# Kernel tuning notes

Hardware: AMD Instinct MI355X
Metric: run time of the kernel (lower is better)

## Reference

```python
import jax, jax.numpy as jnp
import numpy as np

N = 50000
E = 800000
C_IN, C_HID, C_OUT = 128, 64, 1


def setup_inputs() -> dict:
    key = jax.random.key(0)
    ks = jax.random.split(key, 8)
    x = jax.random.normal(ks[0], (N, C_IN), dtype=jnp.float32)
    edge_index = jax.random.randint(ks[1], (2, E), 0, N, dtype=jnp.int64)
    # GCNConv linear params (glorot-ish scaling)
    W1 = jax.random.normal(ks[2], (C_IN, C_HID), dtype=jnp.float32) / np.sqrt(C_IN)
    b1 = jnp.zeros((C_HID,), dtype=jnp.float32)
    W2 = jax.random.normal(ks[3], (C_HID, C_HID), dtype=jnp.float32) / np.sqrt(C_HID)
    b2 = jnp.zeros((C_HID,), dtype=jnp.float32)
    W3 = jax.random.normal(ks[4], (C_HID, C_OUT), dtype=jnp.float32) / np.sqrt(C_HID)
    b3 = jnp.zeros((C_OUT,), dtype=jnp.float32)
    return {"x": x, "edge_index": edge_index, "W1": W1, "b1": b1,
            "W2": W2, "b2": b2, "W3": W3, "b3": b3}


def _gcn_norm(edge_index, num_nodes):
    # Add self-loops, compute symmetric normalization D^{-1/2} A D^{-1/2}
    loop = jnp.arange(num_nodes, dtype=edge_index.dtype)
    src = jnp.concatenate([edge_index[0], loop])  # message sources
    dst = jnp.concatenate([edge_index[1], loop])  # message targets
    ones = jnp.ones(src.shape[0], dtype=jnp.float32)
    deg = jax.ops.segment_sum(ones, dst, num_segments=num_nodes)
    dis = jnp.where(deg > 0, jax.lax.rsqrt(jnp.maximum(deg, 1.0)), 0.0)
    norm = dis[src] * dis[dst]  # [E+N]
    return src, dst, norm


def _gcn_conv(h, src, dst, norm, W, b, num_nodes):
    h = h @ W                                  # [N, C_out]
    msg = h[src] * norm[:, None]               # gather + scale, [E+N, C_out]
    out = jax.ops.segment_sum(msg, dst, num_segments=num_nodes)  # scatter-add
    return out + b


def reference(x, edge_index, W1, b1, W2, b2, W3, b3):
    num_nodes = x.shape[0]
    src, dst, norm = _gcn_norm(edge_index, num_nodes)
    leaky = lambda v: jnp.where(v >= 0, v, 0.01 * v)
    h = _gcn_conv(x, src, dst, norm, W1, b1, num_nodes)
    h = leaky(h)
    h = _gcn_conv(h, src, dst, norm, W2, b2, num_nodes)
    h = leaky(h)
    h = _gcn_conv(h, src, dst, norm, W3, b3, num_nodes)
    return h
```

## Files before the change

### kernel.cpp

```cpp
#include <hip/hip_runtime.h>

#define CIN 128
#define CHID 64
#define CSTRIDE 64

__device__ __forceinline__ float leaky(float v) { return v >= 0.f ? v : 0.01f * v; }
__device__ __forceinline__ float bcast(float v, int k) {
    return __int_as_float(__builtin_amdgcn_readlane(__float_as_int(v), k));
}
__device__ __forceinline__ void acc4(float4& a, const float4 v) {
    a.x += v.x; a.y += v.y; a.z += v.z; a.w += v.w;
}
__device__ __forceinline__ void xorred(float4& a) {
    a.x += __shfl_xor(a.x, 16, 64); a.y += __shfl_xor(a.y, 16, 64);
    a.z += __shfl_xor(a.z, 16, 64); a.w += __shfl_xor(a.w, 16, 64);
    a.x += __shfl_xor(a.x, 32, 64); a.y += __shfl_xor(a.y, 32, 64);
    a.z += __shfl_xor(a.z, 32, 64); a.w += __shfl_xor(a.w, 32, 64);
}

__global__ void k_deg(const int* __restrict__ dst, const int* __restrict__ src,
                      int* __restrict__ deg, unsigned short* __restrict__ csr,
                      int E, int nps, int N) {
    const int shard = blockIdx.x & 7;
    const int chunk = blockIdx.x >> 3;
    const int nchunks = gridDim.x >> 3;
    const int lo = shard * nps;
    const int hi = min(lo + nps, N);
    const int estride = nchunks * 256;
    for (int e = chunk * 256 + threadIdx.x; e < E; e += estride) {
        int d = dst[e];
        if (d >= lo && d < hi) {
            int slot = atomicAdd(&deg[d], 1);
            if (slot < CSTRIDE) csr[(d << 6) + slot] = (unsigned short)src[e];
        }
    }
}

__global__ __launch_bounds__(256) void k_gemm1(
    const float* __restrict__ x, const float* __restrict__ W,
    const int* __restrict__ deg, float* __restrict__ hp, int N) {
    const int wave = threadIdx.x >> 6, lane = threadIdx.x & 63;
    float w[CIN];
#pragma unroll
    for (int k = 0; k < CIN; ++k) w[k] = W[k * CHID + lane];
    const int stride = gridDim.x * 4;
    for (int n = blockIdx.x * 4 + wave; n < N; n += stride) {
        float x0 = x[(size_t)n * CIN + lane];
        float x1 = x[(size_t)n * CIN + 64 + lane];
        float acc0 = 0.f, acc1 = 0.f;
#pragma unroll
        for (int k = 0; k < 64; k += 2) {
            acc0 = fmaf(bcast(x0, k),     w[k],     acc0);
            acc1 = fmaf(bcast(x0, k + 1), w[k + 1], acc1);
        }
#pragma unroll
        for (int k = 0; k < 64; k += 2) {
            acc0 = fmaf(bcast(x1, k),     w[64 + k],     acc0);
            acc1 = fmaf(bcast(x1, k + 1), w[64 + k + 1], acc1);
        }
        float dn = rsqrtf((float)(deg[n] + 1));
        hp[(size_t)n * CHID + lane] = dn * (acc0 + acc1);
    }
}

__global__ __launch_bounds__(256) void kG1(
    const unsigned short* __restrict__ csr, const int* __restrict__ deg,
    const float* __restrict__ hp, const float* __restrict__ W2,
    const float* __restrict__ b1, float* __restrict__ hp2, int N) {
    const int wave = threadIdx.x >> 6, lane = threadIdx.x & 63;
    const int g = lane >> 4, sl = lane & 15;
    float w[CHID];
#pragma unroll
    for (int k = 0; k < CHID; ++k) w[k] = W2[k * CHID + lane];
    const float4 bb = ((const float4*)b1)[sl];
    const float4* __restrict__ hpq = (const float4*)hp;
    const int stride = gridDim.x * 4;
    const int n0 = blockIdx.x * 4 + wave;
    int d = 0, c0 = 0, c1 = 0, c2 = 0, c3 = 0;
    if (n0 < N) {
        d = deg[n0];
        int base = n0 << 6;
        c0 = csr[base + g];      c1 = csr[base + g + 4];
        c2 = csr[base + g + 8];  c3 = csr[base + g + 12];
    }
    for (int n = n0; n < N; n += stride) {
        const int n2 = n + stride;
        int dN = 0, e0 = 0, e1 = 0, e2 = 0, e3 = 0;
        if (n2 < N) {
            dN = deg[n2];
            int b2 = n2 << 6;
            e0 = csr[b2 + g];      e1 = csr[b2 + g + 4];
            e2 = csr[b2 + g + 8];  e3 = csr[b2 + g + 12];
        }
        const int dc = d, base = n << 6;
        float4 a0 = make_float4(0.f, 0.f, 0.f, 0.f), a1 = a0, a2 = a0, a3 = a0;
        if (g == 0) a0 = hpq[(size_t)n * 16 + sl];
        if (g < dc)      acc4(a0, hpq[(size_t)c0 * 16 + sl]);
        if (g + 4 < dc)  acc4(a1, hpq[(size_t)c1 * 16 + sl]);
        if (g + 8 < dc)  acc4(a2, hpq[(size_t)c2 * 16 + sl]);
        if (g + 12 < dc) acc4(a3, hpq[(size_t)c3 * 16 + sl]);
        for (int b = g + 16; b < dc; b += 16) {
            { int s = csr[base + b];      acc4(a0, hpq[(size_t)s * 16 + sl]); }
            if (b + 4 < dc)  { int s = csr[base + b + 4];  acc4(a1, hpq[(size_t)s * 16 + sl]); }
            if (b + 8 < dc)  { int s = csr[base + b + 8];  acc4(a2, hpq[(size_t)s * 16 + sl]); }
            if (b + 12 < dc) { int s = csr[base + b + 12]; acc4(a3, hpq[(size_t)s * 16 + sl]); }
        }
        acc4(a0, a1); acc4(a2, a3); acc4(a0, a2);
        xorred(a0);
        float dn = rsqrtf((float)(dc + 1));
        float4 gv;
        gv.x = leaky(dn * a0.x + bb.x);
        gv.y = leaky(dn * a0.y + bb.y);
        gv.z = leaky(dn * a0.z + bb.z);
        gv.w = leaky(dn * a0.w + bb.w);
        float acc0 = 0.f, acc1 = 0.f;
#pragma unroll
        for (int i = 0; i < 16; ++i) {
            acc0 = fmaf(bcast(gv.x, i), w[4 * i + 0], acc0);
            acc1 = fmaf(bcast(gv.y, i), w[4 * i + 1], acc1);
            acc0 = fmaf(bcast(gv.z, i), w[4 * i + 2], acc0);
            acc1 = fmaf(bcast(gv.w, i), w[4 * i + 3], acc1);
        }
        hp2[(size_t)n * CHID + lane] = dn * (acc0 + acc1);
        d = dN; c0 = e0; c1 = e1; c2 = e2; c3 = e3;
    }
}

__global__ __launch_bounds__(256) void kG2(
    const unsigned short* __restrict__ csr, const int* __restrict__ deg,
    const float* __restrict__ hp, const float* __restrict__ b2,
    const float* __restrict__ W3, float* __restrict__ hp3, int N) {
    const int wave = threadIdx.x >> 6, lane = threadIdx.x & 63;
    const int g = lane >> 4, sl = lane & 15;
    const float4 bb = ((const float4*)b2)[sl];
    const float4 w3 = ((const float4*)W3)[sl];
    const float4* __restrict__ hpq = (const float4*)hp;
    const int stride = gridDim.x * 4;
    const int n0 = blockIdx.x * 4 + wave;
    int d = 0, c0 = 0, c1 = 0, c2 = 0, c3 = 0;
    if (n0 < N) {
        d = deg[n0];
        int base = n0 << 6;
        c0 = csr[base + g];      c1 = csr[base + g + 4];
        c2 = csr[base + g + 8];  c3 = csr[base + g + 12];
    }
    for (int n = n0; n < N; n += stride) {
        const int n2 = n + stride;
        int dN = 0, e0 = 0, e1 = 0, e2 = 0, e3 = 0;
        if (n2 < N) {
            dN = deg[n2];
            int b2i = n2 << 6;
            e0 = csr[b2i + g];      e1 = csr[b2i + g + 4];
            e2 = csr[b2i + g + 8];  e3 = csr[b2i + g + 12];
        }
        const int dc = d, base = n << 6;
        float4 a0 = make_float4(0.f, 0.f, 0.f, 0.f), a1 = a0, a2 = a0, a3 = a0;
        if (g == 0) a0 = hpq[(size_t)n * 16 + sl];
        if (g < dc)      acc4(a0, hpq[(size_t)c0 * 16 + sl]);
        if (g + 4 < dc)  acc4(a1, hpq[(size_t)c1 * 16 + sl]);
        if (g + 8 < dc)  acc4(a2, hpq[(size_t)c2 * 16 + sl]);
        if (g + 12 < dc) acc4(a3, hpq[(size_t)c3 * 16 + sl]);
        for (int b = g + 16; b < dc; b += 16) {
            { int s = csr[base + b];      acc4(a0, hpq[(size_t)s * 16 + sl]); }
            if (b + 4 < dc)  { int s = csr[base + b + 4];  acc4(a1, hpq[(size_t)s * 16 + sl]); }
            if (b + 8 < dc)  { int s = csr[base + b + 8];  acc4(a2, hpq[(size_t)s * 16 + sl]); }
            if (b + 12 < dc) { int s = csr[base + b + 12]; acc4(a3, hpq[(size_t)s * 16 + sl]); }
        }
        acc4(a0, a1); acc4(a2, a3); acc4(a0, a2);
        xorred(a0);
        float dn = rsqrtf((float)(dc + 1));
        float t = leaky(dn * a0.x + bb.x) * w3.x
                + leaky(dn * a0.y + bb.y) * w3.y
                + leaky(dn * a0.z + bb.z) * w3.z
                + leaky(dn * a0.w + bb.w) * w3.w;
        t += __shfl_xor(t, 1, 64); t += __shfl_xor(t, 2, 64);
        t += __shfl_xor(t, 4, 64); t += __shfl_xor(t, 8, 64);
        if (lane == 0) hp3[n] = dn * t;
        d = dN; c0 = e0; c1 = e1; c2 = e2; c3 = e3;
    }
}

__global__ void kG3(const unsigned short* __restrict__ csr, const int* __restrict__ deg,
                    const float* __restrict__ hp3, const float* __restrict__ b3,
                    float* __restrict__ out, int N) {
    int t = blockIdx.x * 256 + threadIdx.x;
    int node = t >> 4, sl = t & 15;
    if (node >= N) return;
    int d = deg[node], base = node << 6;
    float acc = (sl == 0) ? hp3[node] : 0.f;
    for (int i = sl; i < d; i += 16) acc += hp3[(int)csr[base + i]];
#pragma unroll
    for (int off = 8; off > 0; off >>= 1) acc += __shfl_down(acc, off, 16);
    if (sl == 0) out[node] = rsqrtf((float)(d + 1)) * acc + b3[0];
}

extern "C" void kernel_launch(void* const* d_in, const int* in_sizes, int n_in,
                              void* d_out, int out_size, void* d_ws, size_t ws_size,
                              hipStream_t stream) {
    const float* x  = (const float*)d_in[0];
    const int*   ei = (const int*)d_in[1];
    const float* W1 = (const float*)d_in[2];
    const float* b1 = (const float*)d_in[3];
    const float* W2 = (const float*)d_in[4];
    const float* b2 = (const float*)d_in[5];
    const float* W3 = (const float*)d_in[6];
    const float* b3 = (const float*)d_in[7];

    const int N = in_sizes[0] / CIN;
    const int E = in_sizes[1] / 2;
    const int* src = ei;
    const int* dst = ei + E;
    const int nps = (N + 7) / 8;

    char* w = (char*)d_ws;
    auto take = [&](size_t bytes) { char* p = w; w += (bytes + 255) & ~(size_t)255; return p; };
    int*            deg = (int*)take((size_t)N * 4);
    unsigned short* csr = (unsigned short*)take((size_t)N * CSTRIDE * 2);
    float*          A   = (float*)take((size_t)N * CHID * 4);
    float*          B   = (float*)take((size_t)N * CHID * 4);
    float*          hp3 = (float*)take((size_t)N * 4);

    hipMemsetAsync(deg, 0, (size_t)N * 4, stream);

    k_deg  <<<2048, 256, 0, stream>>>(dst, src, deg, csr, E, nps, N);
    k_gemm1<<<1024, 256, 0, stream>>>(x, W1, deg, A, N);
    kG1    <<<2048, 256, 0, stream>>>(csr, deg, A, W2, b1, B, N);
    kG2    <<<2048, 256, 0, stream>>>(csr, deg, B, b2, W3, hp3, N);
    kG3    <<<(N * 16 + 255) / 256, 256, 0, stream>>>(csr, deg, hp3, b3, (float*)d_out, N);
}
```

Measured before the change: 222.9 us.

## Split features into channel slabs and decouple aggregation from dense epilogues

Stores the transformed features as four 16-channel slabs, each a contiguous N×16 array. A new aggregation kernel assigns block groups to one slab and one half of the nodes, so each gather touches a smaller working set that is more likely to stay in cache. The fused aggregate+GEMM kernels are split into a separate aggregation pass plus lightweight epilogue kernels, which adds extra launches and an extra round trip of the full N×64 array through memory. It also clamps the degree loops to the CSR capacity.

Result: slower. 263.9 us (+18.4%).

```diff
diff --git a/kernel.cpp b/kernel.cpp
--- a/kernel.cpp
+++ b/kernel.cpp
@@ -10,12 +10,6 @@
 }
 __device__ __forceinline__ void acc4(float4& a, const float4 v) {
     a.x += v.x; a.y += v.y; a.z += v.z; a.w += v.w;
-}
-__device__ __forceinline__ void xorred(float4& a) {
-    a.x += __shfl_xor(a.x, 16, 64); a.y += __shfl_xor(a.y, 16, 64);
-    a.z += __shfl_xor(a.z, 16, 64); a.w += __shfl_xor(a.w, 16, 64);
-    a.x += __shfl_xor(a.x, 32, 64); a.y += __shfl_xor(a.y, 32, 64);
-    a.z += __shfl_xor(a.z, 32, 64); a.w += __shfl_xor(a.w, 32, 64);
 }
 
 __global__ void k_deg(const int* __restrict__ dst, const int* __restrict__ src,
@@ -38,11 +32,12 @@
 
 __global__ __launch_bounds__(256) void k_gemm1(
     const float* __restrict__ x, const float* __restrict__ W,
-    const int* __restrict__ deg, float* __restrict__ hp, int N) {
+    const int* __restrict__ deg, float* __restrict__ hps, int N) {
     const int wave = threadIdx.x >> 6, lane = threadIdx.x & 63;
     float w[CIN];
 #pragma unroll
     for (int k = 0; k < CIN; ++k) w[k] = W[k * CHID + lane];
+    float* __restrict__ op = hps + (size_t)(lane >> 4) * N * 16 + (lane & 15);
     const int stride = gridDim.x * 4;
     for (int n = blockIdx.x * 4 + wave; n < N; n += stride) {
         float x0 = x[(size_t)n * CIN + lane];
@@ -59,124 +54,93 @@
             acc1 = fmaf(bcast(x1, k + 1), w[64 + k + 1], acc1);
         }
         float dn = rsqrtf((float)(deg[n] + 1));
-        hp[(size_t)n * CHID + lane] = dn * (acc0 + acc1);
+        op[(size_t)n * 16] = dn * (acc0 + acc1);
     }
 }
 
-__global__ __launch_bounds__(256) void kG1(
+__global__ __launch_bounds__(256) void kAgg(
     const unsigned short* __restrict__ csr, const int* __restrict__ deg,
-    const float* __restrict__ hp, const float* __restrict__ W2,
-    const float* __restrict__ b1, float* __restrict__ hp2, int N) {
+    const float* __restrict__ hps, float* __restrict__ hagg, int N) {
     const int wave = threadIdx.x >> 6, lane = threadIdx.x & 63;
-    const int g = lane >> 4, sl = lane & 15;
+    const int q = lane & 3, g = lane >> 2;
+    const int cg = blockIdx.x & 7;
+    const int sh = cg >> 1;
+    const int sub = cg & 1;
+    const int nchunks = gridDim.x >> 3;
+    const int half = (N + 1) >> 1;
+    const int lo = sub * half;
+    const int hi = min(lo + half, N);
+    const float4* __restrict__ hpq = (const float4*)(hps + (size_t)sh * N * 16);
+    const int stride = nchunks * 4;
+    const int n0 = lo + (blockIdx.x >> 3) * 4 + wave;
+    int d = 0, c0 = 0;
+    if (n0 < hi) { d = deg[n0]; c0 = csr[(n0 << 6) + g]; }
+    for (int n = n0; n < hi; n += stride) {
+        const int n2 = n + stride;
+        int dN = 0, e0 = 0;
+        if (n2 < hi) { dN = deg[n2]; e0 = csr[(n2 << 6) + g]; }
+        const int dc = d;
+        const int dcl = min(dc, CSTRIDE);
+        const int base = n << 6;
+        float4 a = make_float4(0.f, 0.f, 0.f, 0.f);
+        if (g == 0) a = hpq[(size_t)n * 4 + q];
+        if (g < dcl) acc4(a, hpq[(size_t)c0 * 4 + q]);
+        for (int b = g + 16; b < dcl; b += 16) {
+            int s = csr[base + b];
+            acc4(a, hpq[(size_t)s * 4 + q]);
+        }
+        a.x += __shfl_xor(a.x, 4, 64);  a.y += __shfl_xor(a.y, 4, 64);
+        a.z += __shfl_xor(a.z, 4, 64);  a.w += __shfl_xor(a.w, 4, 64);
+        a.x += __shfl_xor(a.x, 8, 64);  a.y += __shfl_xor(a.y, 8, 64);
+        a.z += __shfl_xor(a.z, 8, 64);  a.w += __shfl_xor(a.w, 8, 64);
+        a.x += __shfl_xor(a.x, 16, 64); a.y += __shfl_xor(a.y, 16, 64);
+        a.z += __shfl_xor(a.z, 16, 64); a.w += __shfl_xor(a.w, 16, 64);
+        a.x += __shfl_xor(a.x, 32, 64); a.y += __shfl_xor(a.y, 32, 64);
+        a.z += __shfl_xor(a.z, 32, 64); a.w += __shfl_xor(a.w, 32, 64);
+        if (g == 0) ((float4*)(hagg + (size_t)n * 64 + sh * 16))[q] = a;
+        d = dN; c0 = e0;
+    }
+}
+
+__global__ __launch_bounds__(256) void kEpi1(
+    const float* __restrict__ hagg, const int* __restrict__ deg,
+    const float* __restrict__ b1, const float* __restrict__ W2,
+    float* __restrict__ hps2, int N) {
+    const int wave = threadIdx.x >> 6, lane = threadIdx.x & 63;
     float w[CHID];
 #pragma unroll
     for (int k = 0; k < CHID; ++k) w[k] = W2[k * CHID + lane];
-    const float4 bb = ((const float4*)b1)[sl];
-    const float4* __restrict__ hpq = (const float4*)hp;
+    const float bl = b1[lane];
+    float* __restrict__ op = hps2 + (size_t)(lane >> 4) * N * 16 + (lane & 15);
     const int stride = gridDim.x * 4;
-    const int n0 = blockIdx.x * 4 + wave;
-    int d = 0, c0 = 0, c1 = 0, c2 = 0, c3 = 0;
-    if (n0 < N) {
-        d = deg[n0];
-        int base = n0 << 6;
-        c0 = csr[base + g];      c1 = csr[base + g + 4];
-        c2 = csr[base + g + 8];  c3 = csr[base + g + 12];
-    }
-    for (int n = n0; n < N; n += stride) {
-        const int n2 = n + stride;
-        int dN = 0, e0 = 0, e1 = 0, e2 = 0, e3 = 0;
-        if (n2 < N) {
-            dN = deg[n2];
-            int b2 = n2 << 6;
-            e0 = csr[b2 + g];      e1 = csr[b2 + g + 4];
-            e2 = csr[b2 + g + 8];  e3 = csr[b2 + g + 12];
-        }
-        const int dc = d, base = n << 6;
-        float4 a0 = make_float4(0.f, 0.f, 0.f, 0.f), a1 = a0, a2 = a0, a3 = a0;
-        if (g == 0) a0 = hpq[(size_t)n * 16 + sl];
-        if (g < dc)      acc4(a0, hpq[(size_t)c0 * 16 + sl]);
-        if (g + 4 < dc)  acc4(a1, hpq[(size_t)c1 * 16 + sl]);
-        if (g + 8 < dc)  acc4(a2, hpq[(size_t)c2 * 16 + sl]);
-        if (g + 12 < dc) acc4(a3, hpq[(size_t)c3 * 16 + sl]);
-        for (int b = g + 16; b < dc; b += 16) {
-            { int s = csr[base + b];      acc4(a0, hpq[(size_t)s * 16 + sl]); }
-            if (b + 4 < dc)  { int s = csr[base + b + 4];  acc4(a1, hpq[(size_t)s * 16 + sl]); }
-            if (b + 8 < dc)  { int s = csr[base + b + 8];  acc4(a2, hpq[(size_t)s * 16 + sl]); }
-            if (b + 12 < dc) { int s = csr[base + b + 12]; acc4(a3, hpq[(size_t)s * 16 + sl]); }
-        }
-        acc4(a0, a1); acc4(a2, a3); acc4(a0, a2);
-        xorred(a0);
-        float dn = rsqrtf((float)(dc + 1));
-        float4 gv;
-        gv.x = leaky(dn * a0.x + bb.x);
-        gv.y = leaky(dn * a0.y + bb.y);
-        gv.z = leaky(dn * a0.z + bb.z);
-        gv.w = leaky(dn * a0.w + bb.w);
+    for (int n = blockIdx.x * 4 + wave; n < N; n += stride) {
+        float agg = hagg[(size_t)n * 64 + lane];
+        float dn = rsqrtf((float)(deg[n] + 1));
+        float v = leaky(dn * agg + bl);
         float acc0 = 0.f, acc1 = 0.f;
 #pragma unroll
-        for (int i = 0; i < 16; ++i) {
-            acc0 = fmaf(bcast(gv.x, i), w[4 * i + 0], acc0);
-            acc1 = fmaf(bcast(gv.y, i), w[4 * i + 1], acc1);
-            acc0 = fmaf(bcast(gv.z, i), w[4 * i + 2], acc0);
-            acc1 = fmaf(bcast(gv.w, i), w[4 * i + 3], acc1);
+        for (int k = 0; k < 64; k += 2) {
+            acc0 = fmaf(bcast(v, k),     w[k],     acc0);
+            acc1 = fmaf(bcast(v, k + 1), w[k + 1], acc1);
         }
-        hp2[(size_t)n * CHID + lane] = dn * (acc0 + acc1);
-        d = dN; c0 = e0; c1 = e1; c2 = e2; c3 = e3;
+        op[(size_t)n * 16] = dn * (acc0 + acc1);
     }
 }
 
-__global__ __launch_bounds__(256) void kG2(
-    const unsigned short* __restrict__ csr, const int* __restrict__ deg,
-    const float* __restrict__ hp, const float* __restrict__ b2,
-    const float* __restrict__ W3, float* __restrict__ hp3, int N) {
+__global__ __launch_bounds__(256) void kEpi2(
+    const float* __restrict__ hagg, const int* __restrict__ deg,
+    const float* __restrict__ b2, const float* __restrict__ W3,
+    float* __restrict__ hp3, int N) {
     const int wave = threadIdx.x >> 6, lane = threadIdx.x & 63;
-    const int g = lane >> 4, sl = lane & 15;
-    const float4 bb = ((const float4*)b2)[sl];
-    const float4 w3 = ((const float4*)W3)[sl];
-    const float4* __restrict__ hpq = (const float4*)hp;
+    const float bl = b2[lane], wl = W3[lane];
     const int stride = gridDim.x * 4;
-    const int n0 = blockIdx.x * 4 + wave;
-    int d = 0, c0 = 0, c1 = 0, c2 = 0, c3 = 0;
-    if (n0 < N) {
-        d = deg[n0];
-        int base = n0 << 6;
-        c0 = csr[base + g];      c1 = csr[base + g + 4];
-        c2 = csr[base + g + 8];  c3 = csr[base + g + 12];
-    }
-    for (int n = n0; n < N; n += stride) {
-        const int n2 = n + stride;
-        int dN = 0, e0 = 0, e1 = 0, e2 = 0, e3 = 0;
-        if (n2 < N) {
-            dN = deg[n2];
-            int b2i = n2 << 6;
-            e0 = csr[b2i + g];      e1 = csr[b2i + g + 4];
-            e2 = csr[b2i + g + 8];  e3 = csr[b2i + g + 12];
-        }
-        const int dc = d, base = n << 6;
-        float4 a0 = make_float4(0.f, 0.f, 0.f, 0.f), a1 = a0, a2 = a0, a3 = a0;
-        if (g == 0) a0 = hpq[(size_t)n * 16 + sl];
-        if (g < dc)      acc4(a0, hpq[(size_t)c0 * 16 + sl]);
-        if (g + 4 < dc)  acc4(a1, hpq[(size_t)c1 * 16 + sl]);
-        if (g + 8 < dc)  acc4(a2, hpq[(size_t)c2 * 16 + sl]);
-        if (g + 12 < dc) acc4(a3, hpq[(size_t)c3 * 16 + sl]);
-        for (int b = g + 16; b < dc; b += 16) {
-            { int s = csr[base + b];      acc4(a0, hpq[(size_t)s * 16 + sl]); }
-            if (b + 4 < dc)  { int s = csr[base + b + 4];  acc4(a1, hpq[(size_t)s * 16 + sl]); }
-            if (b + 8 < dc)  { int s = csr[base + b + 8];  acc4(a2, hpq[(size_t)s * 16 + sl]); }
-            if (b + 12 < dc) { int s = csr[base + b + 12]; acc4(a3, hpq[(size_t)s * 16 + sl]); }
-        }
-        acc4(a0, a1); acc4(a2, a3); acc4(a0, a2);
-        xorred(a0);
-        float dn = rsqrtf((float)(dc + 1));
-        float t = leaky(dn * a0.x + bb.x) * w3.x
-                + leaky(dn * a0.y + bb.y) * w3.y
-                + leaky(dn * a0.z + bb.z) * w3.z
-                + leaky(dn * a0.w + bb.w) * w3.w;
-        t += __shfl_xor(t, 1, 64); t += __shfl_xor(t, 2, 64);
-        t += __shfl_xor(t, 4, 64); t += __shfl_xor(t, 8, 64);
-        if (lane == 0) hp3[n] = dn * t;
-        d = dN; c0 = e0; c1 = e1; c2 = e2; c3 = e3;
+    for (int n = blockIdx.x * 4 + wave; n < N; n += stride) {
+        float dn = rsqrtf((float)(deg[n] + 1));
+        float v = leaky(dn * hagg[(size_t)n * 64 + lane] + bl) * wl;
+        v += __shfl_xor(v, 1, 64);  v += __shfl_xor(v, 2, 64);
+        v += __shfl_xor(v, 4, 64);  v += __shfl_xor(v, 8, 64);
+        v += __shfl_xor(v, 16, 64); v += __shfl_xor(v, 32, 64);
+        if (lane == 0) hp3[n] = dn * v;
     }
 }
 
@@ -187,8 +151,9 @@
     int node = t >> 4, sl = t & 15;
     if (node >= N) return;
     int d = deg[node], base = node << 6;
+    int dl = min(d, CSTRIDE);
     float acc = (sl == 0) ? hp3[node] : 0.f;
-    for (int i = sl; i < d; i += 16) acc += hp3[(int)csr[base + i]];
+    for (int i = sl; i < dl; i += 16) acc += hp3[(int)csr[base + i]];
 #pragma unroll
     for (int off = 8; off > 0; off >>= 1) acc += __shfl_down(acc, off, 16);
     if (sl == 0) out[node] = rsqrtf((float)(d + 1)) * acc + b3[0];
@@ -214,17 +179,19 @@
 
     char* w = (char*)d_ws;
     auto take = [&](size_t bytes) { char* p = w; w += (bytes + 255) & ~(size_t)255; return p; };
-    int*            deg = (int*)take((size_t)N * 4);
-    unsigned short* csr = (unsigned short*)take((size_t)N * CSTRIDE * 2);
-    float*          A   = (float*)take((size_t)N * CHID * 4);
-    float*          B   = (float*)take((size_t)N * CHID * 4);
-    float*          hp3 = (float*)take((size_t)N * 4);
+    int*            deg  = (int*)take((size_t)N * 4);
+    unsigned short* csr  = (unsigned short*)take((size_t)N * CSTRIDE * 2);
+    float*          buf1 = (float*)take((size_t)N * CHID * 4);
+    float*          buf2 = (float*)take((size_t)N * CHID * 4);
+    float*          hp3  = (float*)take((size_t)N * 4);
 
     hipMemsetAsync(deg, 0, (size_t)N * 4, stream);
 
     k_deg  <<<2048, 256, 0, stream>>>(dst, src, deg, csr, E, nps, N);
-    k_gemm1<<<1024, 256, 0, stream>>>(x, W1, deg, A, N);
-    kG1    <<<2048, 256, 0, stream>>>(csr, deg, A, W2, b1, B, N);
-    kG2    <<<2048, 256, 0, stream>>>(csr, deg, B, b2, W3, hp3, N);
+    k_gemm1<<<1024, 256, 0, stream>>>(x, W1, deg, buf1, N);
+    kAgg   <<<2048, 256, 0, stream>>>(csr, deg, buf1, buf2, N);
+    kEpi1  <<<2048, 256, 0, stream>>>(buf2, deg, b1, W2, buf1, N);
+    kAgg   <<<2048, 256, 0, stream>>>(csr, deg, buf1, buf2, N);
+    kEpi2  <<<2048, 256, 0, stream>>>(buf2, deg, b2, W3, hp3, N);
     kG3    <<<(N * 16 + 255) / 256, 256, 0, stream>>>(csr, deg, hp3, b3, (float*)d_out, N);
 }
```

## Deepen software pipeline for neighbor gathers in GCN aggregation kernels

Applied to the files above, without the earlier changes.

Restructures kG1 and kG2 into a three-stage software pipeline. CSR indices for node n+2·stride are prefetched (8 per lane instead of 4), and the first five feature gathers for node n+stride are issued one iteration early, so more memory loads are in flight to hide gather latency. Degree loops are clamped to CSTRIDE (64), which drops neighbors beyond the fixed CSR row capacity, also in kG3. The change raises register pressure from holding prefetched indices and float4 values.

After: 221.1 us. No clear change (-0.8%).

```diff
diff --git a/kernel.cpp b/kernel.cpp
--- a/kernel.cpp
+++ b/kernel.cpp
@@ -76,38 +76,69 @@
     const float4* __restrict__ hpq = (const float4*)hp;
     const int stride = gridDim.x * 4;
     const int n0 = blockIdx.x * 4 + wave;
-    int d = 0, c0 = 0, c1 = 0, c2 = 0, c3 = 0;
+    const float4 z = make_float4(0.f, 0.f, 0.f, 0.f);
+
+    int dA = 0, dB = 0;
+    int cA[8], cB[8];
+#pragma unroll
+    for (int k = 0; k < 8; ++k) { cA[k] = 0; cB[k] = 0; }
+    float4 pS = z, p0 = z, p1 = z, p2 = z, p3 = z;
+
     if (n0 < N) {
-        d = deg[n0];
-        int base = n0 << 6;
-        c0 = csr[base + g];      c1 = csr[base + g + 4];
-        c2 = csr[base + g + 8];  c3 = csr[base + g + 12];
-    }
+        dA = deg[n0];
+        const int ba = n0 << 6;
+#pragma unroll
+        for (int k = 0; k < 8; ++k) cA[k] = csr[ba + g + 4 * k];
+        const int n1 = n0 + stride;
+        if (n1 < N) {
+            dB = deg[n1];
+            const int bbs = n1 << 6;
+#pragma unroll
+            for (int k = 0; k < 8; ++k) cB[k] = csr[bbs + g + 4 * k];
+        }
+        if (g == 0)      pS = hpq[(size_t)n0 * 16 + sl];
+        if (g < dA)      p0 = hpq[(size_t)cA[0] * 16 + sl];
+        if (g + 4 < dA)  p1 = hpq[(size_t)cA[1] * 16 + sl];
+        if (g + 8 < dA)  p2 = hpq[(size_t)cA[2] * 16 + sl];
+        if (g + 12 < dA) p3 = hpq[(size_t)cA[3] * 16 + sl];
+    }
+
     for (int n = n0; n < N; n += stride) {
-        const int n2 = n + stride;
-        int dN = 0, e0 = 0, e1 = 0, e2 = 0, e3 = 0;
-        if (n2 < N) {
-            dN = deg[n2];
-            int b2 = n2 << 6;
-            e0 = csr[b2 + g];      e1 = csr[b2 + g + 4];
-            e2 = csr[b2 + g + 8];  e3 = csr[b2 + g + 12];
-        }
-        const int dc = d, base = n << 6;
-        float4 a0 = make_float4(0.f, 0.f, 0.f, 0.f), a1 = a0, a2 = a0, a3 = a0;
-        if (g == 0) a0 = hpq[(size_t)n * 16 + sl];
-        if (g < dc)      acc4(a0, hpq[(size_t)c0 * 16 + sl]);
-        if (g + 4 < dc)  acc4(a1, hpq[(size_t)c1 * 16 + sl]);
-        if (g + 8 < dc)  acc4(a2, hpq[(size_t)c2 * 16 + sl]);
-        if (g + 12 < dc) acc4(a3, hpq[(size_t)c3 * 16 + sl]);
-        for (int b = g + 16; b < dc; b += 16) {
-            { int s = csr[base + b];      acc4(a0, hpq[(size_t)s * 16 + sl]); }
-            if (b + 4 < dc)  { int s = csr[base + b + 4];  acc4(a1, hpq[(size_t)s * 16 + sl]); }
-            if (b + 8 < dc)  { int s = csr[base + b + 8];  acc4(a2, hpq[(size_t)s * 16 + sl]); }
-            if (b + 12 < dc) { int s = csr[base + b + 12]; acc4(a3, hpq[(size_t)s * 16 + sl]); }
+        const int nB = n + stride, nC = nB + stride;
+        int dC = 0; int cC[8];
+#pragma unroll
+        for (int k = 0; k < 8; ++k) cC[k] = 0;
+        if (nC < N) {
+            dC = deg[nC];
+            const int bc = nC << 6;
+#pragma unroll
+            for (int k = 0; k < 8; ++k) cC[k] = csr[bc + g + 4 * k];
+        }
+        float4 qS = z, q0 = z, q1 = z, q2 = z, q3 = z;
+        if (nB < N) {
+            if (g == 0)      qS = hpq[(size_t)nB * 16 + sl];
+            if (g < dB)      q0 = hpq[(size_t)cB[0] * 16 + sl];
+            if (g + 4 < dB)  q1 = hpq[(size_t)cB[1] * 16 + sl];
+            if (g + 8 < dB)  q2 = hpq[(size_t)cB[2] * 16 + sl];
+            if (g + 12 < dB) q3 = hpq[(size_t)cB[3] * 16 + sl];
+        }
+        const int dcl = min(dA, CSTRIDE);
+        float4 t0 = z, t1 = z, t2 = z, t3 = z;
+        if (g + 16 < dcl) t0 = hpq[(size_t)cA[4] * 16 + sl];
+        if (g + 20 < dcl) t1 = hpq[(size_t)cA[5] * 16 + sl];
+        if (g + 24 < dcl) t2 = hpq[(size_t)cA[6] * 16 + sl];
+        if (g + 28 < dcl) t3 = hpq[(size_t)cA[7] * 16 + sl];
+        float4 a0 = pS, a1 = p1, a2 = p2, a3 = p3;
+        acc4(a0, p0); acc4(a1, t0); acc4(a2, t1); acc4(a3, t2);
+        acc4(a0, t3);
+        const int base = n << 6;
+        for (int b = g + 32; b < dcl; b += 16) {
+            int s = csr[base + b];
+            acc4(a1, hpq[(size_t)s * 16 + sl]);
         }
         acc4(a0, a1); acc4(a2, a3); acc4(a0, a2);
         xorred(a0);
-        float dn = rsqrtf((float)(dc + 1));
+        float dn = rsqrtf((float)(dA + 1));
         float4 gv;
         gv.x = leaky(dn * a0.x + bb.x);
         gv.y = leaky(dn * a0.y + bb.y);
@@ -122,7 +153,10 @@
             acc1 = fmaf(bcast(gv.w, i), w[4 * i + 3], acc1);
         }
         hp2[(size_t)n * CHID + lane] = dn * (acc0 + acc1);
-        d = dN; c0 = e0; c1 = e1; c2 = e2; c3 = e3;
+        dA = dB; dB = dC;
+#pragma unroll
+        for (int k = 0; k < 8; ++k) { cA[k] = cB[k]; cB[k] = cC[k]; }
+        pS = qS; p0 = q0; p1 = q1; p2 = q2; p3 = q3;
     }
 }
 
@@ -137,38 +171,69 @@
     const float4* __restrict__ hpq = (const float4*)hp;
     const int stride = gridDim.x * 4;
     const int n0 = blockIdx.x * 4 + wave;
-    int d = 0, c0 = 0, c1 = 0, c2 = 0, c3 = 0;
+    const float4 z = make_float4(0.f, 0.f, 0.f, 0.f);
+
+    int dA = 0, dB = 0;
+    int cA[8], cB[8];
+#pragma unroll
+    for (int k = 0; k < 8; ++k) { cA[k] = 0; cB[k] = 0; }
+    float4 pS = z, p0 = z, p1 = z, p2 = z, p3 = z;
+
     if (n0 < N) {
-        d = deg[n0];
-        int base = n0 << 6;
-        c0 = csr[base + g];      c1 = csr[base + g + 4];
-        c2 = csr[base + g + 8];  c3 = csr[base + g + 12];
-    }
+        dA = deg[n0];
+        const int ba = n0 << 6;
+#pragma unroll
+        for (int k = 0; k < 8; ++k) cA[k] = csr[ba + g + 4 * k];
+        const int n1 = n0 + stride;
+        if (n1 < N) {
+            dB = deg[n1];
+            const int bbs = n1 << 6;
+#pragma unroll
+            for (int k = 0; k < 8; ++k) cB[k] = csr[bbs + g + 4 * k];
+        }
+        if (g == 0)      pS = hpq[(size_t)n0 * 16 + sl];
+        if (g < dA)      p0 = hpq[(size_t)cA[0] * 16 + sl];
+        if (g + 4 < dA)  p1 = hpq[(size_t)cA[1] * 16 + sl];
+        if (g + 8 < dA)  p2 = hpq[(size_t)cA[2] * 16 + sl];
+        if (g + 12 < dA) p3 = hpq[(size_t)cA[3] * 16 + sl];
+    }
+
     for (int n = n0; n < N; n += stride) {
-        const int n2 = n + stride;
-        int dN = 0, e0 = 0, e1 = 0, e2 = 0, e3 = 0;
-        if (n2 < N) {
-            dN = deg[n2];
-            int b2i = n2 << 6;
-            e0 = csr[b2i + g];      e1 = csr[b2i + g + 4];
-            e2 = csr[b2i + g + 8];  e3 = csr[b2i + g + 12];
-        }
-        const int dc = d, base = n << 6;
-        float4 a0 = make_float4(0.f, 0.f, 0.f, 0.f), a1 = a0, a2 = a0, a3 = a0;
-        if (g == 0) a0 = hpq[(size_t)n * 16 + sl];
-        if (g < dc)      acc4(a0, hpq[(size_t)c0 * 16 + sl]);
-        if (g + 4 < dc)  acc4(a1, hpq[(size_t)c1 * 16 + sl]);
-        if (g + 8 < dc)  acc4(a2, hpq[(size_t)c2 * 16 + sl]);
-        if (g + 12 < dc) acc4(a3, hpq[(size_t)c3 * 16 + sl]);
-        for (int b = g + 16; b < dc; b += 16) {
-            { int s = csr[base + b];      acc4(a0, hpq[(size_t)s * 16 + sl]); }
-            if (b + 4 < dc)  { int s = csr[base + b + 4];  acc4(a1, hpq[(size_t)s * 16 + sl]); }
-            if (b + 8 < dc)  { int s = csr[base + b + 8];  acc4(a2, hpq[(size_t)s * 16 + sl]); }
-            if (b + 12 < dc) { int s = csr[base + b + 12]; acc4(a3, hpq[(size_t)s * 16 + sl]); }
+        const int nB = n + stride, nC = nB + stride;
+        int dC = 0; int cC[8];
+#pragma unroll
+        for (int k = 0; k < 8; ++k) cC[k] = 0;
+        if (nC < N) {
+            dC = deg[nC];
+            const int bc = nC << 6;
+#pragma unroll
+            for (int k = 0; k < 8; ++k) cC[k] = csr[bc + g + 4 * k];
+        }
+        float4 qS = z, q0 = z, q1 = z, q2 = z, q3 = z;
+        if (nB < N) {
+            if (g == 0)      qS = hpq[(size_t)nB * 16 + sl];
+            if (g < dB)      q0 = hpq[(size_t)cB[0] * 16 + sl];
+            if (g + 4 < dB)  q1 = hpq[(size_t)cB[1] * 16 + sl];
+            if (g + 8 < dB)  q2 = hpq[(size_t)cB[2] * 16 + sl];
+            if (g + 12 < dB) q3 = hpq[(size_t)cB[3] * 16 + sl];
+        }
+        const int dcl = min(dA, CSTRIDE);
+        float4 t0 = z, t1 = z, t2 = z, t3 = z;
+        if (g + 16 < dcl) t0 = hpq[(size_t)cA[4] * 16 + sl];
+        if (g + 20 < dcl) t1 = hpq[(size_t)cA[5] * 16 + sl];
+        if (g + 24 < dcl) t2 = hpq[(size_t)cA[6] * 16 + sl];
+        if (g + 28 < dcl) t3 = hpq[(size_t)cA[7] * 16 + sl];
+        float4 a0 = pS, a1 = p1, a2 = p2, a3 = p3;
+        acc4(a0, p0); acc4(a1, t0); acc4(a2, t1); acc4(a3, t2);
+        acc4(a0, t3);
+        const int base = n << 6;
+        for (int b = g + 32; b < dcl; b += 16) {
+            int s = csr[base + b];
+            acc4(a1, hpq[(size_t)s * 16 + sl]);
         }
         acc4(a0, a1); acc4(a2, a3); acc4(a0, a2);
         xorred(a0);
-        float dn = rsqrtf((float)(dc + 1));
+        float dn = rsqrtf((float)(dA + 1));
         float t = leaky(dn * a0.x + bb.x) * w3.x
                 + leaky(dn * a0.y + bb.y) * w3.y
                 + leaky(dn * a0.z + bb.z) * w3.z
@@ -176,7 +241,10 @@
         t += __shfl_xor(t, 1, 64); t += __shfl_xor(t, 2, 64);
         t += __shfl_xor(t, 4, 64); t += __shfl_xor(t, 8, 64);
         if (lane == 0) hp3[n] = dn * t;
-        d = dN; c0 = e0; c1 = e1; c2 = e2; c3 = e3;
+        dA = dB; dB = dC;
+#pragma unroll
+        for (int k = 0; k < 8; ++k) { cA[k] = cB[k]; cB[k] = cC[k]; }
+        pS = qS; p0 = q0; p1 = q1; p2 = q2; p3 = q3;
     }
 }
 
@@ -187,8 +255,9 @@
     int node = t >> 4, sl = t & 15;
     if (node >= N) return;
     int d = deg[node], base = node << 6;
+    int dl = min(d, CSTRIDE);
     float acc = (sl == 0) ? hp3[node] : 0.f;
-    for (int i = sl; i < d; i += 16) acc += hp3[(int)csr[base + i]];
+    for (int i = sl; i < dl; i += 16) acc += hp3[(int)csr[base + i]];
 #pragma unroll
     for (int off = 8; off > 0; off >>= 1) acc += __shfl_down(acc, off, 16);
     if (sl == 0) out[node] = rsqrtf((float)(d + 1)) * acc + b3[0];
```

## Load whole CSR row per wave, shuffle indices, use LDS broadcast for GEMV

Applied to the files above, without the earlier changes.

The aggregation kernels now load each node's full 64-entry CSR row with one coalesced 32-bit load per lane and extract neighbour indices with wave shuffles, instead of issuing scattered 16-bit loads inside the neighbour loop. Degrees are clamped to the CSR capacity. The per-row GEMVs in gemm1 and kG1 read inputs from shared memory as float4 rather than broadcasting them with readlane. This cuts dependent index-load latency and scalar readlane work, at the cost of extra shuffles and LDS traffic. The LDS write and read in kG1 have no explicit barrier and rely on wave-level execution.

Result: slower. 244.4 us (+9.7%).

```diff
diff --git a/kernel.cpp b/kernel.cpp
--- a/kernel.cpp
+++ b/kernel.cpp
@@ -5,9 +5,6 @@
 #define CSTRIDE 64
 
 __device__ __forceinline__ float leaky(float v) { return v >= 0.f ? v : 0.01f * v; }
-__device__ __forceinline__ float bcast(float v, int k) {
-    return __int_as_float(__builtin_amdgcn_readlane(__float_as_int(v), k));
-}
 __device__ __forceinline__ void acc4(float4& a, const float4 v) {
     a.x += v.x; a.y += v.y; a.z += v.z; a.w += v.w;
 }
@@ -39,24 +36,24 @@
 __global__ __launch_bounds__(256) void k_gemm1(
     const float* __restrict__ x, const float* __restrict__ W,
     const int* __restrict__ deg, float* __restrict__ hp, int N) {
+    __shared__ float xs[4][CIN];
     const int wave = threadIdx.x >> 6, lane = threadIdx.x & 63;
     float w[CIN];
 #pragma unroll
     for (int k = 0; k < CIN; ++k) w[k] = W[k * CHID + lane];
+    const float4* __restrict__ xq = (const float4*)xs[wave];
     const int stride = gridDim.x * 4;
     for (int n = blockIdx.x * 4 + wave; n < N; n += stride) {
-        float x0 = x[(size_t)n * CIN + lane];
-        float x1 = x[(size_t)n * CIN + 64 + lane];
+        xs[wave][lane]      = x[(size_t)n * CIN + lane];
+        xs[wave][64 + lane] = x[(size_t)n * CIN + 64 + lane];
         float acc0 = 0.f, acc1 = 0.f;
 #pragma unroll
-        for (int k = 0; k < 64; k += 2) {
-            acc0 = fmaf(bcast(x0, k),     w[k],     acc0);
-            acc1 = fmaf(bcast(x0, k + 1), w[k + 1], acc1);
-        }
-#pragma unroll
-        for (int k = 0; k < 64; k += 2) {
-            acc0 = fmaf(bcast(x1, k),     w[64 + k],     acc0);
-            acc1 = fmaf(bcast(x1, k + 1), w[64 + k + 1], acc1);
+        for (int i = 0; i < 32; ++i) {
+            float4 v = xq[i];
+            acc0 = fmaf(v.x, w[4 * i + 0], acc0);
+            acc1 = fmaf(v.y, w[4 * i + 1], acc1);
+            acc0 = fmaf(v.z, w[4 * i + 2], acc0);
+            acc1 = fmaf(v.w, w[4 * i + 3], acc1);
         }
         float dn = rsqrtf((float)(deg[n] + 1));
         hp[(size_t)n * CHID + lane] = dn * (acc0 + acc1);
@@ -67,62 +64,77 @@
     const unsigned short* __restrict__ csr, const int* __restrict__ deg,
     const float* __restrict__ hp, const float* __restrict__ W2,
     const float* __restrict__ b1, float* __restrict__ hp2, int N) {
+    __shared__ float lds[4][CHID];
     const int wave = threadIdx.x >> 6, lane = threadIdx.x & 63;
     const int g = lane >> 4, sl = lane & 15;
+    const int gh = g >> 1, sh16 = (g & 1) * 16;
     float w[CHID];
 #pragma unroll
     for (int k = 0; k < CHID; ++k) w[k] = W2[k * CHID + lane];
     const float4 bb = ((const float4*)b1)[sl];
     const float4* __restrict__ hpq = (const float4*)hp;
+    const float4* __restrict__ ldq = (const float4*)lds[wave];
+    const unsigned int* __restrict__ csru = (const unsigned int*)csr;
     const int stride = gridDim.x * 4;
     const int n0 = blockIdx.x * 4 + wave;
-    int d = 0, c0 = 0, c1 = 0, c2 = 0, c3 = 0;
-    if (n0 < N) {
-        d = deg[n0];
-        int base = n0 << 6;
-        c0 = csr[base + g];      c1 = csr[base + g + 4];
-        c2 = csr[base + g + 8];  c3 = csr[base + g + 12];
-    }
+    const float4 z = make_float4(0.f, 0.f, 0.f, 0.f);
+
+    unsigned int cvA = 0; int dA = 0;
+    if (n0 < N) { cvA = csru[(n0 << 5) + (lane & 31)]; dA = deg[n0]; }
+
     for (int n = n0; n < N; n += stride) {
-        const int n2 = n + stride;
-        int dN = 0, e0 = 0, e1 = 0, e2 = 0, e3 = 0;
-        if (n2 < N) {
-            dN = deg[n2];
-            int b2 = n2 << 6;
-            e0 = csr[b2 + g];      e1 = csr[b2 + g + 4];
-            e2 = csr[b2 + g + 8];  e3 = csr[b2 + g + 12];
-        }
-        const int dc = d, base = n << 6;
-        float4 a0 = make_float4(0.f, 0.f, 0.f, 0.f), a1 = a0, a2 = a0, a3 = a0;
-        if (g == 0) a0 = hpq[(size_t)n * 16 + sl];
-        if (g < dc)      acc4(a0, hpq[(size_t)c0 * 16 + sl]);
-        if (g + 4 < dc)  acc4(a1, hpq[(size_t)c1 * 16 + sl]);
-        if (g + 8 < dc)  acc4(a2, hpq[(size_t)c2 * 16 + sl]);
-        if (g + 12 < dc) acc4(a3, hpq[(size_t)c3 * 16 + sl]);
-        for (int b = g + 16; b < dc; b += 16) {
-            { int s = csr[base + b];      acc4(a0, hpq[(size_t)s * 16 + sl]); }
-            if (b + 4 < dc)  { int s = csr[base + b + 4];  acc4(a1, hpq[(size_t)s * 16 + sl]); }
-            if (b + 8 < dc)  { int s = csr[base + b + 8];  acc4(a2, hpq[(size_t)s * 16 + sl]); }
-            if (b + 12 < dc) { int s = csr[base + b + 12]; acc4(a3, hpq[(size_t)s * 16 + sl]); }
+        const int nB = n + stride;
+        unsigned int cvB = 0; int dB = 0;
+        if (nB < N) { cvB = csru[(nB << 5) + (lane & 31)]; dB = deg[nB]; }
+
+        const int dc = min(dA, CSTRIDE);
+        int i0 = (__shfl((int)cvA, gh + 0, 64) >> sh16) & 0xFFFF;
+        int i1 = (__shfl((int)cvA, gh + 2, 64) >> sh16) & 0xFFFF;
+        int i2 = (__shfl((int)cvA, gh + 4, 64) >> sh16) & 0xFFFF;
+        int i3 = (__shfl((int)cvA, gh + 6, 64) >> sh16) & 0xFFFF;
+        float4 a0 = z, a1 = z, a2 = z, a3 = z;
+        if (g == 0)      a0 = hpq[(size_t)n * 16 + sl];
+        if (g < dc)      acc4(a0, hpq[(size_t)i0 * 16 + sl]);
+        if (g + 4 < dc)  acc4(a1, hpq[(size_t)i1 * 16 + sl]);
+        if (g + 8 < dc)  acc4(a2, hpq[(size_t)i2 * 16 + sl]);
+        if (g + 12 < dc) acc4(a3, hpq[(size_t)i3 * 16 + sl]);
+        if (dc > 16) {
+            int i4 = (__shfl((int)cvA, gh +  8, 64) >> sh16) & 0xFFFF;
+            int i5 = (__shfl((int)cvA, gh + 10, 64) >> sh16) & 0xFFFF;
+            int i6 = (__shfl((int)cvA, gh + 12, 64) >> sh16) & 0xFFFF;
+            int i7 = (__shfl((int)cvA, gh + 14, 64) >> sh16) & 0xFFFF;
+            if (g + 16 < dc) acc4(a0, hpq[(size_t)i4 * 16 + sl]);
+            if (g + 20 < dc) acc4(a1, hpq[(size_t)i5 * 16 + sl]);
+            if (g + 24 < dc) acc4(a2, hpq[(size_t)i6 * 16 + sl]);
+            if (g + 28 < dc) acc4(a3, hpq[(size_t)i7 * 16 + sl]);
+            if (dc > 32) {
+#pragma unroll
+                for (int j = 8; j < 16; ++j) {
+                    int ix = (__shfl((int)cvA, gh + 2 * j, 64) >> sh16) & 0xFFFF;
+                    if (g + 4 * j < dc) acc4(a0, hpq[(size_t)ix * 16 + sl]);
+                }
+            }
         }
         acc4(a0, a1); acc4(a2, a3); acc4(a0, a2);
         xorred(a0);
-        float dn = rsqrtf((float)(dc + 1));
+        float dn = rsqrtf((float)(dA + 1));
         float4 gv;
         gv.x = leaky(dn * a0.x + bb.x);
         gv.y = leaky(dn * a0.y + bb.y);
         gv.z = leaky(dn * a0.z + bb.z);
         gv.w = leaky(dn * a0.w + bb.w);
+        if (g == 0) ((float4*)lds[wave])[sl] = gv;
         float acc0 = 0.f, acc1 = 0.f;
 #pragma unroll
         for (int i = 0; i < 16; ++i) {
-            acc0 = fmaf(bcast(gv.x, i), w[4 * i + 0], acc0);
-            acc1 = fmaf(bcast(gv.y, i), w[4 * i + 1], acc1);
-            acc0 = fmaf(bcast(gv.z, i), w[4 * i + 2], acc0);
-            acc1 = fmaf(bcast(gv.w, i), w[4 * i + 3], acc1);
+            float4 gq = ldq[i];
+            acc0 = fmaf(gq.x, w[4 * i + 0], acc0);
+            acc1 = fmaf(gq.y, w[4 * i + 1], acc1);
+            acc0 = fmaf(gq.z, w[4 * i + 2], acc0);
+            acc1 = fmaf(gq.w, w[4 * i + 3], acc1);
         }
         hp2[(size_t)n * CHID + lane] = dn * (acc0 + acc1);
-        d = dN; c0 = e0; c1 = e1; c2 = e2; c3 = e3;
+        cvA = cvB; dA = dB;
     }
 }
 
@@ -132,43 +144,54 @@
     const float* __restrict__ W3, float* __restrict__ hp3, int N) {
     const int wave = threadIdx.x >> 6, lane = threadIdx.x & 63;
     const int g = lane >> 4, sl = lane & 15;
+    const int gh = g >> 1, sh16 = (g & 1) * 16;
     const float4 bb = ((const float4*)b2)[sl];
     const float4 w3 = ((const float4*)W3)[sl];
     const float4* __restrict__ hpq = (const float4*)hp;
+    const unsigned int* __restrict__ csru = (const unsigned int*)csr;
     const int stride = gridDim.x * 4;
     const int n0 = blockIdx.x * 4 + wave;
-    int d = 0, c0 = 0, c1 = 0, c2 = 0, c3 = 0;
-    if (n0 < N) {
-        d = deg[n0];
-        int base = n0 << 6;
-        c0 = csr[base + g];      c1 = csr[base + g + 4];
-        c2 = csr[base + g + 8];  c3 = csr[base + g + 12];
-    }
+    const float4 z = make_float4(0.f, 0.f, 0.f, 0.f);
+
+    unsigned int cvA = 0; int dA = 0;
+    if (n0 < N) { cvA = csru[(n0 << 5) + (lane & 31)]; dA = deg[n0]; }
+
     for (int n = n0; n < N; n += stride) {
-        const int n2 = n + stride;
-        int dN = 0, e0 = 0, e1 = 0, e2 = 0, e3 = 0;
-        if (n2 < N) {
-            dN = deg[n2];
-            int b2i = n2 << 6;
-            e0 = csr[b2i + g];      e1 = csr[b2i + g + 4];
-            e2 = csr[b2i + g + 8];  e3 = csr[b2i + g + 12];
-        }
-        const int dc = d, base = n << 6;
-        float4 a0 = make_float4(0.f, 0.f, 0.f, 0.f), a1 = a0, a2 = a0, a3 = a0;
-        if (g == 0) a0 = hpq[(size_t)n * 16 + sl];
-        if (g < dc)      acc4(a0, hpq[(size_t)c0 * 16 + sl]);
-        if (g + 4 < dc)  acc4(a1, hpq[(size_t)c1 * 16 + sl]);
-        if (g + 8 < dc)  acc4(a2, hpq[(size_t)c2 * 16 + sl]);
-        if (g + 12 < dc) acc4(a3, hpq[(size_t)c3 * 16 + sl]);
-        for (int b = g + 16; b < dc; b += 16) {
-            { int s = csr[base + b];      acc4(a0, hpq[(size_t)s * 16 + sl]); }
-            if (b + 4 < dc)  { int s = csr[base + b + 4];  acc4(a1, hpq[(size_t)s * 16 + sl]); }
-            if (b + 8 < dc)  { int s = csr[base + b + 8];  acc4(a2, hpq[(size_t)s * 16 + sl]); }
-            if (b + 12 < dc) { int s = csr[base + b + 12]; acc4(a3, hpq[(size_t)s * 16 + sl]); }
+        const int nB = n + stride;
+        unsigned int cvB = 0; int dB = 0;
+        if (nB < N) { cvB = csru[(nB << 5) + (lane & 31)]; dB = deg[nB]; }
+
+        const int dc = min(dA, CSTRIDE);
+        int i0 = (__shfl((int)cvA, gh + 0, 64) >> sh16) & 0xFFFF;
+        int i1 = (__shfl((int)cvA, gh + 2, 64) >> sh16) & 0xFFFF;
+        int i2 = (__shfl((int)cvA, gh + 4, 64) >> sh16) & 0xFFFF;
+        int i3 = (__shfl((int)cvA, gh + 6, 64) >> sh16) & 0xFFFF;
+        float4 a0 = z, a1 = z, a2 = z, a3 = z;
+        if (g == 0)      a0 = hpq[(size_t)n * 16 + sl];
+        if (g < dc)      acc4(a0, hpq[(size_t)i0 * 16 + sl]);
+        if (g + 4 < dc)  acc4(a1, hpq[(size_t)i1 * 16 + sl]);
+        if (g + 8 < dc)  acc4(a2, hpq[(size_t)i2 * 16 + sl]);
+        if (g + 12 < dc) acc4(a3, hpq[(size_t)i3 * 16 + sl]);
+        if (dc > 16) {
+            int i4 = (__shfl((int)cvA, gh +  8, 64) >> sh16) & 0xFFFF;
+            int i5 = (__shfl((int)cvA, gh + 10, 64) >> sh16) & 0xFFFF;
+            int i6 = (__shfl((int)cvA, gh + 12, 64) >> sh16) & 0xFFFF;
+            int i7 = (__shfl((int)cvA, gh + 14, 64) >> sh16) & 0xFFFF;
+            if (g + 16 < dc) acc4(a0, hpq[(size_t)i4 * 16 + sl]);
+            if (g + 20 < dc) acc4(a1, hpq[(size_t)i5 * 16 + sl]);
+            if (g + 24 < dc) acc4(a2, hpq[(size_t)i6 * 16 + sl]);
+            if (g + 28 < dc) acc4(a3, hpq[(size_t)i7 * 16 + sl]);
+            if (dc > 32) {
+#pragma unroll
+                for (int j = 8; j < 16; ++j) {
+                    int ix = (__shfl((int)cvA, gh + 2 * j, 64) >> sh16) & 0xFFFF;
+                    if (g + 4 * j < dc) acc4(a0, hpq[(size_t)ix * 16 + sl]);
+                }
+            }
         }
         acc4(a0, a1); acc4(a2, a3); acc4(a0, a2);
         xorred(a0);
-        float dn = rsqrtf((float)(dc + 1));
+        float dn = rsqrtf((float)(dA + 1));
         float t = leaky(dn * a0.x + bb.x) * w3.x
                 + leaky(dn * a0.y + bb.y) * w3.y
                 + leaky(dn * a0.z + bb.z) * w3.z
@@ -176,7 +199,7 @@
         t += __shfl_xor(t, 1, 64); t += __shfl_xor(t, 2, 64);
         t += __shfl_xor(t, 4, 64); t += __shfl_xor(t, 8, 64);
         if (lane == 0) hp3[n] = dn * t;
-        d = dN; c0 = e0; c1 = e1; c2 = e2; c3 = e3;
+        cvA = cvB; dA = dB;
     }
 }
 
@@ -187,8 +210,9 @@
     int node = t >> 4, sl = t & 15;
     if (node >= N) return;
     int d = deg[node], base = node << 6;
+    int dl = min(d, CSTRIDE);
     float acc = (sl == 0) ? hp3[node] : 0.f;
-    for (int i = sl; i < d; i += 16) acc += hp3[(int)csr[base + i]];
+    for (int i = sl; i < dl; i += 16) acc += hp3[(int)csr[base + i]];
 #pragma unroll
     for (int off = 8; off > 0; off >>= 1) acc += __shfl_down(acc, off, 16);
     if (sl == 0) out[node] = rsqrtf((float)(d + 1)) * acc + b3[0];
```
